# Kernel tuning notes

Hardware: AMD Instinct MI355X
Metric: run time of the kernel (lower is better)

## Reference

```python
import jax, jax.numpy as jnp
import numpy as np

NUM_USERS = 100000
NUM_ITEMS = 50000
NUM_NODES = NUM_USERS + NUM_ITEMS
EMBED_DIM = 64
NUM_LAYERS = 3
NUM_EDGES = 1200000


def setup_inputs() -> dict:
    key = jax.random.key(0)
    k1, k2 = jax.random.split(key)
    edge_index = jax.random.randint(k1, (2, NUM_EDGES), 0, NUM_NODES, dtype=jnp.int32)
    # xavier_uniform for [N, D]
    limit = float(np.sqrt(6.0 / (NUM_NODES + EMBED_DIM)))
    embedding = jax.random.uniform(k2, (NUM_NODES, EMBED_DIM), dtype=jnp.float32,
                                   minval=-limit, maxval=limit)
    return {"edge_index": edge_index, "embedding": embedding}


def reference(edge_index, embedding):
    n = embedding.shape[0]
    row, col = edge_index[0], edge_index[1]
    ones = jnp.ones((edge_index.shape[1],), dtype=embedding.dtype)
    deg_row = jax.ops.segment_sum(ones, row, num_segments=n)
    deg_col = jax.ops.segment_sum(ones, col, num_segments=n)
    # deg^-0.5 with inf (deg==0) -> 0
    inv_row = jnp.where(deg_row > 0, jax.lax.rsqrt(jnp.maximum(deg_row, 1e-30)), 0.0)
    inv_col = jnp.where(deg_col > 0, jax.lax.rsqrt(jnp.maximum(deg_col, 1e-30)), 0.0)
    norm = (inv_row[row] * inv_col[col])[:, None]  # [E, 1]

    x = embedding
    accum = x
    for _ in range(NUM_LAYERS):
        # gather source embeddings, scale by symmetric norm, scatter-add at target
        msgs = norm * x[row]                       # [E, D]
        x = jax.ops.segment_sum(msgs, col, num_segments=n)
        accum = accum + x
    final = accum / jnp.asarray(NUM_LAYERS + 1, dtype=embedding.dtype)
    return final[:NUM_USERS], final[NUM_USERS:]
```

## Files before the change

kernel.cpp:

```cpp
#include <hip/hip_runtime.h>
#include <hip/hip_fp16.h>


constexpr int NUM_USERS = 100000;
constexpr int NUM_ITEMS = 50000;
constexpr int N_NODES   = NUM_USERS + NUM_ITEMS;
constexpr int EMBED_DIM = 64;
constexpr int NUM_EDGES = 1200000;
constexpr int SHIFT = 9;
constexpr int BSZ   = 1 << SHIFT;
constexpr int NBUCK = (N_NODES + BSZ - 1) >> SHIFT;
constexpr int CAPC  = 4480;
constexpr int EPB   = 1024;
constexpr int P1_BLOCKS = (NUM_EDGES + EPB - 1) / EPB;

__global__ void __launch_bounds__(256)
pass1_bin(const int4* __restrict__ row4, const int4* __restrict__ col4,
          int* __restrict__ gcur_c, int* __restrict__ gcur_r,
          unsigned int* __restrict__ binned_c, unsigned short* __restrict__ binned_r) {
    __shared__ int hist_c[NBUCK], hist_r[NBUCK], cur_c[NBUCK], cur_r[NBUCK];
    int t = threadIdx.x;
    for (int i = t; i < NBUCK; i += 256) { hist_c[i] = 0; hist_r[i] = 0; }
    __syncthreads();
    int base4 = blockIdx.x * (EPB / 4);
    constexpr int NV = NUM_EDGES / 4;
    {
        int v = base4 + t;
        if (v < NV) {
            int4 c = col4[v];
            atomicAdd(&hist_c[c.x >> SHIFT], 1);
            atomicAdd(&hist_c[c.y >> SHIFT], 1);
            atomicAdd(&hist_c[c.z >> SHIFT], 1);
            atomicAdd(&hist_c[c.w >> SHIFT], 1);
            int4 r = row4[v];
            atomicAdd(&hist_r[r.x >> SHIFT], 1);
            atomicAdd(&hist_r[r.y >> SHIFT], 1);
            atomicAdd(&hist_r[r.z >> SHIFT], 1);
            atomicAdd(&hist_r[r.w >> SHIFT], 1);
        }
    }
    __syncthreads();
    for (int i = t; i < NBUCK; i += 256) {
        cur_c[i] = atomicAdd(&gcur_c[i], hist_c[i]);
        cur_r[i] = atomicAdd(&gcur_r[i], hist_r[i]);
    }
    __syncthreads();
    {
        int v = base4 + t;
        if (v < NV) {
            int4 c = col4[v];
            int4 r = row4[v];
            int cc[4] = {c.x, c.y, c.z, c.w};
            int rr[4] = {r.x, r.y, r.z, r.w};
#pragma unroll
            for (int q = 0; q < 4; ++q) {
                int dc = cc[q] >> SHIFT;
                int sc = atomicAdd(&cur_c[dc], 1);
                if (sc < CAPC)
                    binned_c[dc * CAPC + sc] =
                        ((unsigned)(cc[q] & (BSZ - 1)) << 18) | (unsigned)rr[q];
                int dr = rr[q] >> SHIFT;
                int sr = atomicAdd(&cur_r[dr], 1);
                if (sr < CAPC)
                    binned_r[dr * CAPC + sr] = (unsigned short)(rr[q] & (BSZ - 1));
            }
        }
    }
}

__global__ void __launch_bounds__(256)
pass2_place(const int* __restrict__ gcur_c, const int* __restrict__ gcur_r,
            const unsigned int* __restrict__ binned_c, const unsigned short* __restrict__ binned_r,
            int* __restrict__ sorted_idx, int* __restrict__ packed_pc,
            float* __restrict__ inv_col, float* __restrict__ inv_row) {
    __shared__ int hist[BSZ];
    __shared__ int partial[256];
    int t = threadIdx.x;
    hist[t] = 0; hist[t + 256] = 0;
    __syncthreads();
    int b = blockIdx.x;
    if (b < NBUCK) {
        int n = gcur_c[b]; if (n > CAPC) n = CAPC;
        const unsigned int* src = binned_c + b * CAPC;
        for (int i = t; i < n; i += 256) atomicAdd(&hist[src[i] >> 18], 1);
        int s = 0;
        for (int i = t; i < b; i += 256) s += gcur_c[i];
        partial[t] = s;
        __syncthreads();
        for (int off = 128; off > 0; off >>= 1) {
            if (t < off) partial[t] += partial[t + off];
            __syncthreads();
        }
        int bucket_base = partial[0];
        __syncthreads();
        int v0 = hist[t * 2], v1 = hist[t * 2 + 1];
        int sum = v0 + v1;
        partial[t] = sum; __syncthreads();
        for (int off = 1; off < 256; off <<= 1) {
            int tv = (t >= off) ? partial[t - off] : 0;
            __syncthreads();
            partial[t] += tv;
            __syncthreads();
        }
        int excl = partial[t] - sum;
        int o0 = excl, o1 = excl + v0;
        hist[t * 2] = o0; hist[t * 2 + 1] = o1;
        int c0 = (b << SHIFT) | (t * 2);
        if (c0 < N_NODES) {
            packed_pc[c0] = ((bucket_base + o0) << 7) | v0;
            inv_col[c0] = (v0 > 0) ? rsqrtf((float)v0) : 0.0f;
        }
        int c1 = c0 + 1;
        if (c1 < N_NODES) {
            packed_pc[c1] = ((bucket_base + o1) << 7) | v1;
            inv_col[c1] = (v1 > 0) ? rsqrtf((float)v1) : 0.0f;
        }
        __syncthreads();
        for (int i = t; i < n; i += 256) {
            unsigned int w = src[i];
            int lc = w >> 18;
            int r  = (int)(w & 0x3FFFFu);
            int slot = atomicAdd(&hist[lc], 1);
            sorted_idx[bucket_base + slot] = r;
        }
    } else {
        int bb = b - NBUCK;
        int n = gcur_r[bb]; if (n > CAPC) n = CAPC;
        const unsigned short* src = binned_r + bb * CAPC;
        for (int i = t; i < n; i += 256) atomicAdd(&hist[src[i]], 1);
        __syncthreads();
        int c0 = (bb << SHIFT) | (t * 2);
        int v0 = hist[t * 2], v1 = hist[t * 2 + 1];
        if (c0 < N_NODES)     inv_row[c0] = (v0 > 0) ? rsqrtf((float)v0) : 0.0f;
        if (c0 + 1 < N_NODES) inv_row[c0 + 1] = (v1 > 0) ? rsqrtf((float)v1) : 0.0f;
    }
}

__global__ void init_y_kernel(const float* __restrict__ inv_row,
                              const float2* __restrict__ emb2, __half2* __restrict__ y0) {
    int i = blockIdx.x * blockDim.x + threadIdx.x;
    if (i < N_NODES * (EMBED_DIM / 2)) {
        float w = inv_row[i >> 5];
        float2 e = emb2[i];
        y0[i] = __floats2half2_rn(w * e.x, w * e.y);
    }
}

__global__ void __launch_bounds__(256, 8)
layer_kernel(const int* __restrict__ packed_pc,
             const int* __restrict__ sorted_idx,
             const float* __restrict__ inv_row,
             const float* __restrict__ inv_col,
             const int4* __restrict__ y_src,
             int4* __restrict__ y_dst,
             float4* __restrict__ out4,
             const float4* __restrict__ emb4,
             int mode) {
    int wid  = (blockIdx.x * blockDim.x + threadIdx.x) >> 6;
    int lane = threadIdx.x & 63;
    if (wid >= N_NODES) return;
    int d4 = lane & 7;
    int e  = lane >> 3;
    int packed = packed_pc[wid];
    int cnt = packed & 127;
    int ptr = packed >> 7;
    int lidx = (cnt > 0) ? (ptr + ((lane < cnt) ? lane : 0)) : 0;
    int idx = sorted_idx[lidx];

    int obase = wid * 16 + d4 * 2;
    float4 o0, o1;
    if (e == 1) {
        const float4* src = (mode == 0) ? emb4 : (const float4*)out4;
        o0 = src[obase];
        o1 = src[obase + 1];
    }

    float f[8] = {0.f, 0.f, 0.f, 0.f, 0.f, 0.f, 0.f, 0.f};
    for (int j = 0; j < cnt; j += 8) {
        int s = __shfl(idx, j + e);
        int4 v = y_src[s * 8 + d4];
        if (j + e < cnt) {
            float2 a0 = __half22float2(*reinterpret_cast<const __half2*>(&v.x));
            float2 a1 = __half22float2(*reinterpret_cast<const __half2*>(&v.y));
            float2 a2 = __half22float2(*reinterpret_cast<const __half2*>(&v.z));
            float2 a3 = __half22float2(*reinterpret_cast<const __half2*>(&v.w));
            f[0] += a0.x; f[1] += a0.y; f[2] += a1.x; f[3] += a1.y;
            f[4] += a2.x; f[5] += a2.y; f[6] += a3.x; f[7] += a3.y;
        }
    }
#pragma unroll
    for (int k = 0; k < 8; ++k) {
        f[k] += __shfl_xor(f[k], 8);
        f[k] += __shfl_xor(f[k], 16);
        f[k] += __shfl_xor(f[k], 32);
    }
    float invc = inv_col[wid];
#pragma unroll
    for (int k = 0; k < 8; ++k) f[k] *= invc;

    if (mode != 2) {
        if (e == 0) {
            float w = inv_row[wid];
            __half2 p0 = __floats2half2_rn(w * f[0], w * f[1]);
            __half2 p1 = __floats2half2_rn(w * f[2], w * f[3]);
            __half2 p2 = __floats2half2_rn(w * f[4], w * f[5]);
            __half2 p3 = __floats2half2_rn(w * f[6], w * f[7]);
            int4 st;
            st.x = *reinterpret_cast<int*>(&p0);
            st.y = *reinterpret_cast<int*>(&p1);
            st.z = *reinterpret_cast<int*>(&p2);
            st.w = *reinterpret_cast<int*>(&p3);
            y_dst[wid * 8 + d4] = st;
        } else if (e == 1) {
            o0.x += f[0]; o0.y += f[1]; o0.z += f[2]; o0.w += f[3];
            o1.x += f[4]; o1.y += f[5]; o1.z += f[6]; o1.w += f[7];
            out4[obase]     = o0;
            out4[obase + 1] = o1;
        }
    } else if (e == 1) {
        o0.x = (o0.x + f[0]) * 0.25f; o0.y = (o0.y + f[1]) * 0.25f;
        o0.z = (o0.z + f[2]) * 0.25f; o0.w = (o0.w + f[3]) * 0.25f;
        o1.x = (o1.x + f[4]) * 0.25f; o1.y = (o1.y + f[5]) * 0.25f;
        o1.z = (o1.z + f[6]) * 0.25f; o1.w = (o1.w + f[7]) * 0.25f;
        out4[obase]     = o0;
        out4[obase + 1] = o1;
    }
}

extern "C" void kernel_launch(void* const* d_in, const int* in_sizes, int n_in,
                              void* d_out, int out_size, void* d_ws, size_t ws_size,
                              hipStream_t stream) {
    const int*   edge_index = (const int*)d_in[0];
    const float* embedding  = (const float*)d_in[1];
    const int* row = edge_index;
    const int* col = edge_index + NUM_EDGES;
    float* out = (float*)d_out;

    char* ws = (char*)d_ws;
    auto align_up = [](size_t v) { return (v + 255) & ~size_t(255); };
    size_t off = 0;
    int* gcur_c     = (int*)(ws + off); off = align_up(off + sizeof(int) * NBUCK);
    int* gcur_r     = (int*)(ws + off); off = align_up(off + sizeof(int) * NBUCK);
    size_t cursor_bytes = off;
    int* packed_pc  = (int*)(ws + off); off = align_up(off + sizeof(int) * N_NODES);
    float* inv_row  = (float*)(ws + off); off = align_up(off + sizeof(float) * N_NODES);
    float* inv_col  = (float*)(ws + off); off = align_up(off + sizeof(float) * N_NODES);
    int* sorted_idx = (int*)(ws + off); off = align_up(off + sizeof(int) * NUM_EDGES);
    __half2* ya     = (__half2*)(ws + off); off = align_up(off + sizeof(__half2) * N_NODES * 32);
    __half2* yb     = (__half2*)(ws + off); off = align_up(off + sizeof(__half2) * N_NODES * 32);
    unsigned int*   binned_c = (unsigned int*)yb;
    unsigned short* binned_r = (unsigned short*)((char*)yb + align_up(sizeof(unsigned int) * NBUCK * CAPC));

    hipMemsetAsync(gcur_c, 0, cursor_bytes, stream);
    pass1_bin<<<P1_BLOCKS, 256, 0, stream>>>((const int4*)row, (const int4*)col,
                                             gcur_c, gcur_r, binned_c, binned_r);
    pass2_place<<<2 * NBUCK, 256, 0, stream>>>(gcur_c, gcur_r, binned_c, binned_r,
                                               sorted_idx, packed_pc, inv_col, inv_row);
    {
        int n2 = N_NODES * 32;
        int threads = 256, blocks = (n2 + threads - 1) / threads;
        init_y_kernel<<<blocks, threads, 0, stream>>>(inv_row, (const float2*)embedding, ya);
    }
    {
        int threads = 256;
        int blocks = (N_NODES * 64 + threads - 1) / threads;
        layer_kernel<<<blocks, threads, 0, stream>>>(packed_pc, sorted_idx, inv_row, inv_col,
                                                     (const int4*)ya, (int4*)yb, (float4*)out,
                                                     (const float4*)embedding, 0);
        layer_kernel<<<blocks, threads, 0, stream>>>(packed_pc, sorted_idx, inv_row, inv_col,
                                                     (const int4*)yb, (int4*)ya, (float4*)out,
                                                     (const float4*)embedding, 1);
        layer_kernel<<<blocks, threads, 0, stream>>>(packed_pc, sorted_idx, inv_row, inv_col,
                                                     (const int4*)ya, (int4*)yb , (float4*)out,
                                                     (const float4*)embedding, 2);
    }
}
```

Baseline: 313.2 us.

## Add padded per-node neighbor table to skip dependent index load in layers

pass2 now also writes up to 16 source indices per destination node into a fixed-stride table. For nodes with at most 16 in-edges, the layer kernel reads its neighbor indices straight from this table instead of first reading packed_pc and then sorted_idx, which removes a dependent load from the start of every wavefront. Pass1 also handles four times as many edges per block, which cuts the number of global cursor atomics, and init_y now processes float4 vectors. In exchange, pass2 writes an extra 16-int table per node and each layer reads 64 bytes of indices per node, which adds memory traffic.

Result: faster. 277.9 us (-11.3%).

```diff
diff --git a/kernel.cpp b/kernel.cpp
--- a/kernel.cpp
+++ b/kernel.cpp
@@ -11,8 +11,9 @@
 constexpr int BSZ   = 1 << SHIFT;
 constexpr int NBUCK = (N_NODES + BSZ - 1) >> SHIFT;
 constexpr int CAPC  = 4480;
-constexpr int EPB   = 1024;
+constexpr int EPB   = 4096;
 constexpr int P1_BLOCKS = (NUM_EDGES + EPB - 1) / EPB;
+constexpr int FIXCAP = 16;
 
 __global__ void __launch_bounds__(256)
 pass1_bin(const int4* __restrict__ row4, const int4* __restrict__ col4,
@@ -24,8 +25,8 @@
     __syncthreads();
     int base4 = blockIdx.x * (EPB / 4);
     constexpr int NV = NUM_EDGES / 4;
-    {
-        int v = base4 + t;
+    for (int k = 0; k < EPB / 1024; ++k) {
+        int v = base4 + k * 256 + t;
         if (v < NV) {
             int4 c = col4[v];
             atomicAdd(&hist_c[c.x >> SHIFT], 1);
@@ -45,8 +46,8 @@
         cur_r[i] = atomicAdd(&gcur_r[i], hist_r[i]);
     }
     __syncthreads();
-    {
-        int v = base4 + t;
+    for (int k = 0; k < EPB / 1024; ++k) {
+        int v = base4 + k * 256 + t;
         if (v < NV) {
             int4 c = col4[v];
             int4 r = row4[v];
@@ -71,9 +72,10 @@
 __global__ void __launch_bounds__(256)
 pass2_place(const int* __restrict__ gcur_c, const int* __restrict__ gcur_r,
             const unsigned int* __restrict__ binned_c, const unsigned short* __restrict__ binned_r,
-            int* __restrict__ sorted_idx, int* __restrict__ packed_pc,
+            int* __restrict__ sorted_idx, int* __restrict__ fixed_idx, int* __restrict__ packed_pc,
             float* __restrict__ inv_col, float* __restrict__ inv_row) {
     __shared__ int hist[BSZ];
+    __shared__ int obase[BSZ];
     __shared__ int partial[256];
     int t = threadIdx.x;
     hist[t] = 0; hist[t + 256] = 0;
@@ -105,6 +107,7 @@
         int excl = partial[t] - sum;
         int o0 = excl, o1 = excl + v0;
         hist[t * 2] = o0; hist[t * 2 + 1] = o1;
+        obase[t * 2] = o0; obase[t * 2 + 1] = o1;
         int c0 = (b << SHIFT) | (t * 2);
         if (c0 < N_NODES) {
             packed_pc[c0] = ((bucket_base + o0) << 7) | v0;
@@ -122,6 +125,9 @@
             int r  = (int)(w & 0x3FFFFu);
             int slot = atomicAdd(&hist[lc], 1);
             sorted_idx[bucket_base + slot] = r;
+            int within = slot - obase[lc];
+            if (within < FIXCAP)
+                fixed_idx[(((b << SHIFT) | lc) << 4) + within] = r;
         }
     } else {
         int bb = b - NBUCK;
@@ -137,18 +143,21 @@
 }
 
 __global__ void init_y_kernel(const float* __restrict__ inv_row,
-                              const float2* __restrict__ emb2, __half2* __restrict__ y0) {
+                              const float4* __restrict__ emb4, int2* __restrict__ y0) {
     int i = blockIdx.x * blockDim.x + threadIdx.x;
-    if (i < N_NODES * (EMBED_DIM / 2)) {
-        float w = inv_row[i >> 5];
-        float2 e = emb2[i];
-        y0[i] = __floats2half2_rn(w * e.x, w * e.y);
+    if (i < N_NODES * (EMBED_DIM / 4)) {
+        float w = inv_row[i >> 4];
+        float4 e = emb4[i];
+        __half2 h0 = __floats2half2_rn(w * e.x, w * e.y);
+        __half2 h1 = __floats2half2_rn(w * e.z, w * e.w);
+        y0[i] = make_int2(*reinterpret_cast<int*>(&h0), *reinterpret_cast<int*>(&h1));
     }
 }
 
 __global__ void __launch_bounds__(256, 8)
 layer_kernel(const int* __restrict__ packed_pc,
              const int* __restrict__ sorted_idx,
+             const int* __restrict__ fixed_idx,
              const float* __restrict__ inv_row,
              const float* __restrict__ inv_col,
              const int4* __restrict__ y_src,
@@ -161,18 +170,24 @@
     if (wid >= N_NODES) return;
     int d4 = lane & 7;
     int e  = lane >> 3;
+
+    int rec    = fixed_idx[(wid << 4) | (lane & 15)];
     int packed = packed_pc[wid];
-    int cnt = packed & 127;
-    int ptr = packed >> 7;
-    int lidx = (cnt > 0) ? (ptr + ((lane < cnt) ? lane : 0)) : 0;
-    int idx = sorted_idx[lidx];
-
+    float invc = inv_col[wid];
+    float invr = inv_row[wid];
     int obase = wid * 16 + d4 * 2;
     float4 o0, o1;
     if (e == 1) {
         const float4* src = (mode == 0) ? emb4 : (const float4*)out4;
         o0 = src[obase];
         o1 = src[obase + 1];
+    }
+
+    int cnt = packed & 127;
+    int ptr = packed >> 7;
+    int idx = ((lane & 15) < cnt) ? rec : 0;
+    if (cnt > FIXCAP) {
+        idx = sorted_idx[ptr + ((lane < cnt) ? lane : 0)];
     }
 
     float f[8] = {0.f, 0.f, 0.f, 0.f, 0.f, 0.f, 0.f, 0.f};
@@ -194,17 +209,15 @@
         f[k] += __shfl_xor(f[k], 16);
         f[k] += __shfl_xor(f[k], 32);
     }
-    float invc = inv_col[wid];
 #pragma unroll
     for (int k = 0; k < 8; ++k) f[k] *= invc;
 
     if (mode != 2) {
         if (e == 0) {
-            float w = inv_row[wid];
-            __half2 p0 = __floats2half2_rn(w * f[0], w * f[1]);
-            __half2 p1 = __floats2half2_rn(w * f[2], w * f[3]);
-            __half2 p2 = __floats2half2_rn(w * f[4], w * f[5]);
-            __half2 p3 = __floats2half2_rn(w * f[6], w * f[7]);
+            __half2 p0 = __floats2half2_rn(invr * f[0], invr * f[1]);
+            __half2 p1 = __floats2half2_rn(invr * f[2], invr * f[3]);
+            __half2 p2 = __floats2half2_rn(invr * f[4], invr * f[5]);
+            __half2 p3 = __floats2half2_rn(invr * f[6], invr * f[7]);
             int4 st;
             st.x = *reinterpret_cast<int*>(&p0);
             st.y = *reinterpret_cast<int*>(&p1);
@@ -246,6 +259,7 @@
     float* inv_row  = (float*)(ws + off); off = align_up(off + sizeof(float) * N_NODES);
     float* inv_col  = (float*)(ws + off); off = align_up(off + sizeof(float) * N_NODES);
     int* sorted_idx = (int*)(ws + off); off = align_up(off + sizeof(int) * NUM_EDGES);
+    int* fixed_idx  = (int*)(ws + off); off = align_up(off + sizeof(int) * N_NODES * FIXCAP);
     __half2* ya     = (__half2*)(ws + off); off = align_up(off + sizeof(__half2) * N_NODES * 32);
     __half2* yb     = (__half2*)(ws + off); off = align_up(off + sizeof(__half2) * N_NODES * 32);
     unsigned int*   binned_c = (unsigned int*)yb;
@@ -255,22 +269,22 @@
     pass1_bin<<<P1_BLOCKS, 256, 0, stream>>>((const int4*)row, (const int4*)col,
                                              gcur_c, gcur_r, binned_c, binned_r);
     pass2_place<<<2 * NBUCK, 256, 0, stream>>>(gcur_c, gcur_r, binned_c, binned_r,
-                                               sorted_idx, packed_pc, inv_col, inv_row);
+                                               sorted_idx, fixed_idx, packed_pc, inv_col, inv_row);
     {
-        int n2 = N_NODES * 32;
-        int threads = 256, blocks = (n2 + threads - 1) / threads;
-        init_y_kernel<<<blocks, threads, 0, stream>>>(inv_row, (const float2*)embedding, ya);
+        int n4 = N_NODES * 16;
+        int threads = 256, blocks = (n4 + threads - 1) / threads;
+        init_y_kernel<<<blocks, threads, 0, stream>>>(inv_row, (const float4*)embedding, (int2*)ya);
     }
     {
         int threads = 256;
         int blocks = (N_NODES * 64 + threads - 1) / threads;
-        layer_kernel<<<blocks, threads, 0, stream>>>(packed_pc, sorted_idx, inv_row, inv_col,
+        layer_kernel<<<blocks, threads, 0, stream>>>(packed_pc, sorted_idx, fixed_idx, inv_row, inv_col,
                                                      (const int4*)ya, (int4*)yb, (float4*)out,
                                                      (const float4*)embedding, 0);
-        layer_kernel<<<blocks, threads, 0, stream>>>(packed_pc, sorted_idx, inv_row, inv_col,
+        layer_kernel<<<blocks, threads, 0, stream>>>(packed_pc, sorted_idx, fixed_idx, inv_row, inv_col,
                                                      (const int4*)yb, (int4*)ya, (float4*)out,
                                                      (const float4*)embedding, 1);
-        layer_kernel<<<blocks, threads, 0, stream>>>(packed_pc, sorted_idx, inv_row, inv_col,
+        layer_kernel<<<blocks, threads, 0, stream>>>(packed_pc, sorted_idx, fixed_idx, inv_row, inv_col,
                                                      (const int4*)ya, (int4*)yb , (float4*)out,
                                                      (const float4*)embedding, 2);
     }
```
